# Performance work log

Measured on AMD Instinct MI355X. Metric: run time of the kernel, lower is better.

The kernel has to match this reference:

```python
import jax, jax.numpy as jnp
import numpy as np
import math

B, S, D, H = 2, 2048, 1024, 16
HD = D // H  # head_dim = 64

def setup_inputs() -> dict:
    key = jax.random.key(0)
    ks = jax.random.split(key, 11)
    def n(k, shape, scale=1.0):
        return jax.random.normal(k, shape, dtype=jnp.float32) * scale
    w_scale = 1.0 / math.sqrt(D)
    return {
        "q": n(ks[0], (B, S, D)),
        "k": n(ks[1], (B, S, D)),
        "v": n(ks[2], (B, S, D)),
        "WQ_w": n(ks[3], (D, D), w_scale),
        "WQ_b": n(ks[4], (D,), 0.01),
        "WK_w": n(ks[5], (D, D), w_scale),
        "WK_b": n(ks[6], (D,), 0.01),
        "WV_w": n(ks[7], (D, D), w_scale),
        "WV_b": n(ks[8], (D,), 0.01),
        "Wout_w": n(ks[9], (D, D), w_scale),
        "Wout_b": n(ks[10], (D,), 0.01),
    }

def reference(q, k, v, WQ_w, WQ_b, WK_w, WK_b, WV_w, WV_b, Wout_w, Wout_b):
    b, s, _ = k.shape
    # QKV projections (torch Linear: x @ W.T + b; here weights stored [in, out])
    qh = (q @ WQ_w + WQ_b).reshape(b, -1, H, HD).transpose(0, 2, 1, 3)  # [b,h,s,hd]
    kh = (k @ WK_w + WK_b).reshape(b, -1, H, HD).transpose(0, 2, 1, 3)
    vh = (v @ WV_w + WV_b).reshape(b, -1, H, HD).transpose(0, 2, 1, 3)
    # naive attention: full [b,h,s,s] score matrix
    scores = jnp.einsum("bhqd,bhkd->bhqk", qh, kh) / math.sqrt(HD)
    attn = jax.nn.softmax(scores, axis=-1)
    out = jnp.einsum("bhqk,bhkd->bhqd", attn, vh)
    concat = out.transpose(0, 2, 1, 3).reshape(b, -1, H * HD)  # [b,s,inner_dim]
    return concat @ Wout_w + Wout_b
```

## Files before the change

kernel.cpp:

```cpp
#include <hip/hip_runtime.h>
#include <hip/hip_bf16.h>
#include <stdint.h>

typedef __attribute__((ext_vector_type(8))) short bf16x8;
typedef __attribute__((ext_vector_type(4))) short short4v;
typedef __attribute__((ext_vector_type(4))) float f32x4;

#define MFMA16x16x32 __builtin_amdgcn_mfma_f32_16x16x32_bf16

__device__ __forceinline__ short f2b(float f) {
  union { float f; uint32_t u; } x;
  x.f = f;
  uint32_t u = x.u;
  uint32_t r = (u + 0x7FFFu + ((u >> 16) & 1u)) >> 16;
  return (short)(uint16_t)r;
}

__device__ __forceinline__ uint32_t cvt_pk_bf16(float lo, float hi) {
  uint32_t r;
  asm volatile("v_cvt_pk_bf16_f32 %0, %1, %2" : "=v"(r) : "v"(lo), "v"(hi));
  return r;
}
__device__ __forceinline__ float exp2_fast(float x) {
  float r;
  asm volatile("v_exp_f32 %0, %1" : "=v"(r) : "v"(x));
  return r;
}
__device__ __forceinline__ bf16x8 cvt8(const float4 a, const float4 b) {
  union { uint32_t u[4]; bf16x8 v; } o;
  o.u[0] = cvt_pk_bf16(a.x, a.y);
  o.u[1] = cvt_pk_bf16(a.z, a.w);
  o.u[2] = cvt_pk_bf16(b.x, b.y);
  o.u[3] = cvt_pk_bf16(b.z, b.w);
  return o.v;
}

__device__ __forceinline__ void async_copy16(const void* g, void* l) {
  __builtin_amdgcn_global_load_lds(
      (const __attribute__((address_space(1))) void*)g,
      (__attribute__((address_space(3))) void*)l, 16, 0, 0);
}

__global__ void transpose4_kernel(const float* __restrict__ W0,
                                  const float* __restrict__ W1,
                                  const float* __restrict__ W2,
                                  const float* __restrict__ W3,
                                  short* __restrict__ Wt) {
  __shared__ short tile[64][72];
  const int mat = blockIdx.z;
  const float* W = (mat == 0) ? W0 : (mat == 1) ? W1 : (mat == 2) ? W2 : W3;
  short* Wo = Wt + (size_t)mat * 1024 * 1024;
  const int r0 = blockIdx.y * 64;
  const int c0 = blockIdx.x * 64;
  const int t = threadIdx.x;
#pragma unroll
  for (int i = 0; i < 4; ++i) {
    const int lin = i * 1024 + t * 4;
    const int r = lin >> 6, c = lin & 63;
    const float4 v = *(const float4*)&W[(size_t)(r0 + r) * 1024 + c0 + c];
    tile[r][c + 0] = f2b(v.x);
    tile[r][c + 1] = f2b(v.y);
    tile[r][c + 2] = f2b(v.z);
    tile[r][c + 3] = f2b(v.w);
  }
  __syncthreads();
#pragma unroll
  for (int i = 0; i < 2; ++i) {
    const int lin = i * 2048 + t * 8;
    const int r = lin >> 6, c = lin & 63;
    bf16x8 ov;
#pragma unroll
    for (int jj = 0; jj < 8; ++jj) ov[jj] = tile[c + jj][r];
    *(bf16x8*)&Wo[(size_t)(c0 + r) * 1024 + r0 + c] = ov;
  }
}

__launch_bounds__(256, 2)
__global__ void gemm_qkv_kernel(const float* __restrict__ A0,
                                const float* __restrict__ A1,
                                const float* __restrict__ A2,
                                const short* __restrict__ WtBase,
                                const float* __restrict__ b0,
                                const float* __restrict__ b1,
                                const float* __restrict__ b2,
                                short* __restrict__ C0,
                                short* __restrict__ C1,
                                short* __restrict__ Vt) {
  const int K = 1024;
  __shared__ short As[128 * 64];
  __shared__ short Bs[128 * 64];

  const int y = blockIdx.y;
  const float* A = (y == 0) ? A0 : (y == 1) ? A1 : A2;
  const short* Wt = WtBase + (size_t)y * 1024 * 1024;
  const float* bias = (y == 0) ? b0 : (y == 1) ? b1 : b2;

  const int tm = blockIdx.x & 31;
  const int tn = blockIdx.x >> 5;
  const int m0 = tm * 128, n0 = tn * 128;

  const int tid = threadIdx.x;
  const int lane = tid & 63;
  const int w = tid >> 6;
  const int wr = w >> 1, wc = w & 1;

  const int srow = lane >> 3;
  const int schunk = lane & 7;

  f32x4 acc[4][4] = {};

  for (int kt = 0; kt < 16; ++kt) {
    const int k0 = kt * 64;
#pragma unroll
    for (int i = 0; i < 4; ++i) {
      const int ri = w * 4 + i;
      const int row = ri * 8 + srow;
      const int gch = schunk ^ (row & 7);
      async_copy16(Wt + (size_t)(n0 + row) * K + (k0 + gch * 8), &Bs[ri * 512]);
    }
#pragma unroll
    for (int i = 0; i < 4; ++i) {
      const int ri = w * 4 + i;
      const int row = ri * 8 + srow;
      const float* src = A + (size_t)(m0 + row) * 1024 + k0 + schunk * 8;
      const float4 a = *(const float4*)src;
      const float4 b = *(const float4*)(src + 4);
      *(bf16x8*)&As[row * 64 + ((schunk ^ (row & 7)) << 3)] = cvt8(a, b);
    }
    __syncthreads();
#pragma unroll
    for (int kk = 0; kk < 2; ++kk) {
      bf16x8 af[4], bfr[4];
#pragma unroll
      for (int x = 0; x < 4; ++x) {
        const int gch = kk * 4 + (lane >> 4);
        const int rowA = wr * 64 + x * 16 + (lane & 15);
        af[x] = *(const bf16x8*)&As[rowA * 64 + ((gch ^ (rowA & 7)) << 3)];
        const int rowB = wc * 64 + x * 16 + (lane & 15);
        bfr[x] = *(const bf16x8*)&Bs[rowB * 64 + ((gch ^ (rowB & 7)) << 3)];
      }
#pragma unroll
      for (int x = 0; x < 4; ++x)
#pragma unroll
        for (int yy = 0; yy < 4; ++yy)
          acc[x][yy] = MFMA16x16x32(af[x], bfr[yy], acc[x][yy], 0, 0, 0);
    }
    __syncthreads();
  }

  short* Cout = (y == 0) ? C0 : C1;
#pragma unroll
  for (int x = 0; x < 4; ++x) {
    const int rbase = m0 + wr * 64 + x * 16 + ((lane >> 4) << 2);
#pragma unroll
    for (int yy = 0; yy < 4; ++yy) {
      const int col = n0 + wc * 64 + yy * 16 + (lane & 15);
      const float bv = bias[col];
      if (y == 2) {
        const int b = rbase >> 11, s = rbase & 2047;
        const int hh = col >> 6, d = col & 63;
        short4v pack;
#pragma unroll
        for (int r = 0; r < 4; ++r) pack[r] = f2b(acc[x][yy][r] + bv);
        *(short4v*)&Vt[((size_t)(b * 16 + hh) * 64 + d) * 2048 + s] = pack;
      } else {
#pragma unroll
        for (int r = 0; r < 4; ++r)
          Cout[(size_t)(rbase + r) * 1024 + col] = f2b(acc[x][yy][r] + bv);
      }
    }
  }
}

__launch_bounds__(256, 2)
__global__ void gemm_out_kernel(const short* __restrict__ A,
                                const short* __restrict__ Wt,
                                const float* __restrict__ bias,
                                float* __restrict__ C) {
  const int N = 1024, K = 1024;
  __shared__ short As[128 * 64];
  __shared__ short Bs[128 * 64];

  const int tm = blockIdx.x & 31;
  const int tn = blockIdx.x >> 5;
  const int m0 = tm * 128, n0 = tn * 128;

  const int tid = threadIdx.x;
  const int lane = tid & 63;
  const int w = tid >> 6;
  const int wr = w >> 1, wc = w & 1;
  const int srow = lane >> 3, schunk = lane & 7;

  f32x4 acc[4][4] = {};

  for (int kt = 0; kt < 16; ++kt) {
    const int k0 = kt * 64;
#pragma unroll
    for (int i = 0; i < 4; ++i) {
      const int ri = w * 4 + i;
      const int row = ri * 8 + srow;
      const int gch = schunk ^ (row & 7);
      async_copy16(A + (size_t)(m0 + row) * K + (k0 + gch * 8), &As[ri * 512]);
      async_copy16(Wt + (size_t)(n0 + row) * K + (k0 + gch * 8), &Bs[ri * 512]);
    }
    __syncthreads();
#pragma unroll
    for (int kk = 0; kk < 2; ++kk) {
      bf16x8 af[4], bfr[4];
#pragma unroll
      for (int x = 0; x < 4; ++x) {
        const int gch = kk * 4 + (lane >> 4);
        const int rowA = wr * 64 + x * 16 + (lane & 15);
        af[x] = *(const bf16x8*)&As[rowA * 64 + ((gch ^ (rowA & 7)) << 3)];
        const int rowB = wc * 64 + x * 16 + (lane & 15);
        bfr[x] = *(const bf16x8*)&Bs[rowB * 64 + ((gch ^ (rowB & 7)) << 3)];
      }
#pragma unroll
      for (int x = 0; x < 4; ++x)
#pragma unroll
        for (int yy = 0; yy < 4; ++yy)
          acc[x][yy] = MFMA16x16x32(af[x], bfr[yy], acc[x][yy], 0, 0, 0);
    }
    __syncthreads();
  }

#pragma unroll
  for (int x = 0; x < 4; ++x) {
    const int rbase = m0 + wr * 64 + x * 16 + ((lane >> 4) << 2);
#pragma unroll
    for (int yy = 0; yy < 4; ++yy) {
      const int col = n0 + wc * 64 + yy * 16 + (lane & 15);
      const float bv = bias[col];
#pragma unroll
      for (int r = 0; r < 4; ++r)
        C[(size_t)(rbase + r) * N + col] = acc[x][yy][r] + bv;
    }
  }
}

__launch_bounds__(256, 2)
__global__ void attn_kernel(const short* __restrict__ qh,
                            const short* __restrict__ kh,
                            const short* __restrict__ Vt,
                            short* __restrict__ concat) {
  const int S = 2048;
  const float CL2 = 0.18033688011112042f;
  __shared__ short Ks[2][64 * 64];
  __shared__ short Vs[2][64 * 64];
  __shared__ short Ps[4 * 32 * 64];

  const int qb = blockIdx.x;
  const int h = blockIdx.y;
  const int b = blockIdx.z;
  const int tid = threadIdx.x, lane = tid & 63, w = tid >> 6;
  const int hi = lane >> 4, cc = lane & 15;

  const size_t rowbase = (size_t)b * S;
  const int q0 = qb * 128 + w * 32;

  bf16x8 qf[2][2];
#pragma unroll
  for (int aq = 0; aq < 2; ++aq)
#pragma unroll
    for (int kk = 0; kk < 2; ++kk) {
      const int col = h * 64 + kk * 32 + hi * 8;
      qf[aq][kk] =
          *(const bf16x8*)&qh[(rowbase + q0 + aq * 16 + cc) * 1024 + col];
    }

  f32x4 oacc[2][4] = {};
  float l[2] = {0.f, 0.f};

  const short* Vth = Vt + (size_t)(b * 16 + h) * 64 * 2048;
  short* Pw = &Ps[w * 2048];
  const int srow = lane >> 3, schunk = lane & 7;
  const int e0 = (cc >> 3) & 1;

#pragma unroll
  for (int i = 0; i < 2; ++i) {
    const int ri = w * 2 + i;
    const int row = ri * 8 + srow;
    const int gch = schunk ^ (row & 7);
    async_copy16(&kh[(rowbase + row) * 1024 + h * 64 + gch * 8], &Ks[0][ri * 512]);
    async_copy16(&Vth[(size_t)row * 2048 + gch * 8], &Vs[0][ri * 512]);
  }
  __syncthreads();

  for (int t = 0; t < S / 64; ++t) {
    const int cur = t & 1;
    if (t + 1 < S / 64) {
      const int kv0 = (t + 1) * 64;
#pragma unroll
      for (int i = 0; i < 2; ++i) {
        const int ri = w * 2 + i;
        const int row = ri * 8 + srow;
        const int gch = schunk ^ (row & 7);
        async_copy16(&kh[(rowbase + kv0 + row) * 1024 + h * 64 + gch * 8],
                     &Ks[cur ^ 1][ri * 512]);
        async_copy16(&Vth[(size_t)row * 2048 + kv0 + gch * 8],
                     &Vs[cur ^ 1][ri * 512]);
      }
    }

    f32x4 sacc[2][4] = {};
#pragma unroll
    for (int kk = 0; kk < 2; ++kk) {
      bf16x8 kf[4];
#pragma unroll
      for (int n = 0; n < 4; ++n) {
        const int row = n * 16 + cc;
        const int ch = (kk * 4 + hi) ^ (cc & 7);
        kf[n] = *(const bf16x8*)&Ks[cur][row * 64 + (ch << 3)];
      }
#pragma unroll
      for (int aq = 0; aq < 2; ++aq)
#pragma unroll
        for (int n = 0; n < 4; ++n)
          sacc[aq][n] = MFMA16x16x32(kf[n], qf[aq][kk], sacc[aq][n], 0, 0, 0);
    }

#pragma unroll
    for (int aq = 0; aq < 2; ++aq) {
      const int qrow = aq * 16 + cc;
#pragma unroll
      for (int n = 0; n < 4; ++n) {
        const float p0 = exp2_fast(sacc[aq][n][0] * CL2);
        const float p1 = exp2_fast(sacc[aq][n][1] * CL2);
        const float p2 = exp2_fast(sacc[aq][n][2] * CL2);
        const float p3 = exp2_fast(sacc[aq][n][3] * CL2);
        l[aq] += (p0 + p1) + (p2 + p3);
        const uint32_t u0 = cvt_pk_bf16(p0, p1);
        const uint32_t u1 = cvt_pk_bf16(p2, p3);
        const int chunk = (2 * n + (hi >> 1)) ^ (cc & 7);
        const int base = qrow * 64 + (chunk << 3) + ((hi & 1) << 2);
        *(uint32_t*)&Pw[base + (e0 << 1)] = e0 ? u1 : u0;
        *(uint32_t*)&Pw[base + ((e0 ^ 1) << 1)] = e0 ? u0 : u1;
      }
    }

#pragma unroll
    for (int kvh = 0; kvh < 2; ++kvh) {
      const int ch = (kvh * 4 + hi) ^ (cc & 7);
      bf16x8 pf[2], vf[4];
#pragma unroll
      for (int aq = 0; aq < 2; ++aq)
        pf[aq] = *(const bf16x8*)&Pw[(aq * 16 + cc) * 64 + (ch << 3)];
#pragma unroll
      for (int n = 0; n < 4; ++n) {
        const int row = n * 16 + cc;
        vf[n] = *(const bf16x8*)&Vs[cur][row * 64 + (ch << 3)];
      }
#pragma unroll
      for (int aq = 0; aq < 2; ++aq)
#pragma unroll
        for (int n = 0; n < 4; ++n)
          oacc[aq][n] = MFMA16x16x32(vf[n], pf[aq], oacc[aq][n], 0, 0, 0);
    }
    __syncthreads();
  }

#pragma unroll
  for (int aq = 0; aq < 2; ++aq) {
    float lv = l[aq];
    lv += __shfl_xor(lv, 16);
    lv += __shfl_xor(lv, 32);
    const float inv = 1.0f / lv;
    const size_t grow = rowbase + q0 + aq * 16 + cc;
#pragma unroll
    for (int n = 0; n < 4; ++n)
#pragma unroll
      for (int r = 0; r < 4; ++r) {
        const int d = n * 16 + hi * 4 + r;
        concat[grow * 1024 + h * 64 + d] = f2b(oacc[aq][n][r] * inv);
      }
  }
}

extern "C" void kernel_launch(void* const* d_in, const int* in_sizes, int n_in,
                              void* d_out, int out_size, void* d_ws, size_t ws_size,
                              hipStream_t stream) {
  const float* q = (const float*)d_in[0];
  const float* k = (const float*)d_in[1];
  const float* v = (const float*)d_in[2];
  const float* WQ = (const float*)d_in[3];
  const float* bQ = (const float*)d_in[4];
  const float* WK = (const float*)d_in[5];
  const float* bK = (const float*)d_in[6];
  const float* WV = (const float*)d_in[7];
  const float* bV = (const float*)d_in[8];
  const float* WO = (const float*)d_in[9];
  const float* bO = (const float*)d_in[10];

  char* ws = (char*)d_ws;
  const size_t MB = 1024 * 1024;
  short* Wt = (short*)ws;
  short* qh = (short*)(ws + 8 * MB);
  short* kh = (short*)(ws + 16 * MB);
  short* Vt = (short*)(ws + 24 * MB);
  short* concat = (short*)(ws + 32 * MB);

  transpose4_kernel<<<dim3(16, 16, 4), 256, 0, stream>>>(WQ, WK, WV, WO, Wt);
  gemm_qkv_kernel<<<dim3(256, 3), 256, 0, stream>>>(
      q, k, v, Wt, bQ, bK, bV, qh, kh, Vt);
  attn_kernel<<<dim3(16, 16, 2), 256, 0, stream>>>(qh, kh, Vt, concat);
  gemm_out_kernel<<<256, 256, 0, stream>>>(concat, Wt + 3 * MB, bO,
                                           (float*)d_out);
}
```

Measured before the change: 123.5 us.

## Load GEMM A operand directly to registers and double-buffer weight tiles in LDS

In both the QKV and output projection GEMMs, the A operand is no longer staged through shared memory. Each wave now reads its MFMA fragments straight from global memory (converting fp32 to bf16 in registers for the QKV kernel). The weight tile is double-buffered in LDS, with the next tile prefetched asynchronously after the barrier, so the trailing __syncthreads per k-step can be removed. The aim is to cut LDS traffic and barriers and to overlap weight loads with MFMA work. The cost is that the two waves sharing a row block now fetch the same A data twice from global/L2, and A load latency is no longer hidden by any prefetch.

```diff
diff --git a/kernel.cpp b/kernel.cpp
--- a/kernel.cpp
+++ b/kernel.cpp
@@ -87,8 +87,7 @@
                                 short* __restrict__ C1,
                                 short* __restrict__ Vt) {
   const int K = 1024;
-  __shared__ short As[128 * 64];
-  __shared__ short Bs[128 * 64];
+  __shared__ short Bs[2][128 * 64];
 
   const int y = blockIdx.y;
   const float* A = (y == 0) ? A0 : (y == 1) ? A1 : A2;
@@ -103,58 +102,73 @@
   const int lane = tid & 63;
   const int w = tid >> 6;
   const int wr = w >> 1, wc = w & 1;
+  const int hi = lane >> 4, cc = lane & 15;
 
   const int srow = lane >> 3;
   const int schunk = lane & 7;
 
   f32x4 acc[4][4] = {};
 
+#pragma unroll
+  for (int i = 0; i < 4; ++i) {
+    const int ri = w * 4 + i;
+    const int row = ri * 8 + srow;
+    const int gch = schunk ^ (row & 7);
+    async_copy16(Wt + (size_t)(n0 + row) * K + gch * 8, &Bs[0][ri * 512]);
+  }
+
   for (int kt = 0; kt < 16; ++kt) {
+    const int cur = kt & 1;
     const int k0 = kt * 64;
-#pragma unroll
-    for (int i = 0; i < 4; ++i) {
-      const int ri = w * 4 + i;
-      const int row = ri * 8 + srow;
-      const int gch = schunk ^ (row & 7);
-      async_copy16(Wt + (size_t)(n0 + row) * K + (k0 + gch * 8), &Bs[ri * 512]);
-    }
-#pragma unroll
-    for (int i = 0; i < 4; ++i) {
-      const int ri = w * 4 + i;
-      const int row = ri * 8 + srow;
-      const float* src = A + (size_t)(m0 + row) * 1024 + k0 + schunk * 8;
-      const float4 a = *(const float4*)src;
-      const float4 b = *(const float4*)(src + 4);
-      *(bf16x8*)&As[row * 64 + ((schunk ^ (row & 7)) << 3)] = cvt8(a, b);
-    }
+
+    bf16x8 af[2][4];
+#pragma unroll
+    for (int kk = 0; kk < 2; ++kk)
+#pragma unroll
+      for (int x = 0; x < 4; ++x) {
+        const float* src = A + (size_t)(m0 + wr * 64 + x * 16 + cc) * 1024 +
+                           k0 + kk * 32 + hi * 8;
+        af[kk][x] = cvt8(*(const float4*)src, *(const float4*)(src + 4));
+      }
+
     __syncthreads();
+
+    if (kt < 15) {
+      const int k1 = k0 + 64;
+#pragma unroll
+      for (int i = 0; i < 4; ++i) {
+        const int ri = w * 4 + i;
+        const int row = ri * 8 + srow;
+        const int gch = schunk ^ (row & 7);
+        async_copy16(Wt + (size_t)(n0 + row) * K + (k1 + gch * 8),
+                     &Bs[cur ^ 1][ri * 512]);
+      }
+    }
+
 #pragma unroll
     for (int kk = 0; kk < 2; ++kk) {
-      bf16x8 af[4], bfr[4];
-#pragma unroll
-      for (int x = 0; x < 4; ++x) {
-        const int gch = kk * 4 + (lane >> 4);
-        const int rowA = wr * 64 + x * 16 + (lane & 15);
-        af[x] = *(const bf16x8*)&As[rowA * 64 + ((gch ^ (rowA & 7)) << 3)];
-        const int rowB = wc * 64 + x * 16 + (lane & 15);
-        bfr[x] = *(const bf16x8*)&Bs[rowB * 64 + ((gch ^ (rowB & 7)) << 3)];
+      bf16x8 bfr[4];
+#pragma unroll
+      for (int yy = 0; yy < 4; ++yy) {
+        const int gch = kk * 4 + hi;
+        const int rowB = wc * 64 + yy * 16 + cc;
+        bfr[yy] = *(const bf16x8*)&Bs[cur][rowB * 64 + ((gch ^ (rowB & 7)) << 3)];
       }
 #pragma unroll
       for (int x = 0; x < 4; ++x)
 #pragma unroll
         for (int yy = 0; yy < 4; ++yy)
-          acc[x][yy] = MFMA16x16x32(af[x], bfr[yy], acc[x][yy], 0, 0, 0);
-    }
-    __syncthreads();
+          acc[x][yy] = MFMA16x16x32(af[kk][x], bfr[yy], acc[x][yy], 0, 0, 0);
+    }
   }
 
   short* Cout = (y == 0) ? C0 : C1;
 #pragma unroll
   for (int x = 0; x < 4; ++x) {
-    const int rbase = m0 + wr * 64 + x * 16 + ((lane >> 4) << 2);
+    const int rbase = m0 + wr * 64 + x * 16 + (hi << 2);
 #pragma unroll
     for (int yy = 0; yy < 4; ++yy) {
-      const int col = n0 + wc * 64 + yy * 16 + (lane & 15);
+      const int col = n0 + wc * 64 + yy * 16 + cc;
       const float bv = bias[col];
       if (y == 2) {
         const int b = rbase >> 11, s = rbase & 2047;
@@ -178,8 +192,7 @@
                                 const float* __restrict__ bias,
                                 float* __restrict__ C) {
   const int N = 1024, K = 1024;
-  __shared__ short As[128 * 64];
-  __shared__ short Bs[128 * 64];
+  __shared__ short Bs[2][128 * 64];
 
   const int tm = blockIdx.x & 31;
   const int tn = blockIdx.x >> 5;
@@ -189,47 +202,68 @@
   const int lane = tid & 63;
   const int w = tid >> 6;
   const int wr = w >> 1, wc = w & 1;
+  const int hi = lane >> 4, cc = lane & 15;
   const int srow = lane >> 3, schunk = lane & 7;
 
   f32x4 acc[4][4] = {};
 
+#pragma unroll
+  for (int i = 0; i < 4; ++i) {
+    const int ri = w * 4 + i;
+    const int row = ri * 8 + srow;
+    const int gch = schunk ^ (row & 7);
+    async_copy16(Wt + (size_t)(n0 + row) * K + gch * 8, &Bs[0][ri * 512]);
+  }
+
   for (int kt = 0; kt < 16; ++kt) {
+    const int cur = kt & 1;
     const int k0 = kt * 64;
-#pragma unroll
-    for (int i = 0; i < 4; ++i) {
-      const int ri = w * 4 + i;
-      const int row = ri * 8 + srow;
-      const int gch = schunk ^ (row & 7);
-      async_copy16(A + (size_t)(m0 + row) * K + (k0 + gch * 8), &As[ri * 512]);
-      async_copy16(Wt + (size_t)(n0 + row) * K + (k0 + gch * 8), &Bs[ri * 512]);
-    }
+
+    bf16x8 af[2][4];
+#pragma unroll
+    for (int kk = 0; kk < 2; ++kk)
+#pragma unroll
+      for (int x = 0; x < 4; ++x)
+        af[kk][x] = *(const bf16x8*)&A[(size_t)(m0 + wr * 64 + x * 16 + cc) * 1024 +
+                                       k0 + kk * 32 + hi * 8];
+
     __syncthreads();
+
+    if (kt < 15) {
+      const int k1 = k0 + 64;
+#pragma unroll
+      for (int i = 0; i < 4; ++i) {
+        const int ri = w * 4 + i;
+        const int row = ri * 8 + srow;
+        const int gch = schunk ^ (row & 7);
+        async_copy16(Wt + (size_t)(n0 + row) * K + (k1 + gch * 8),
+                     &Bs[cur ^ 1][ri * 512]);
+      }
+    }
+
 #pragma unroll
     for (int kk = 0; kk < 2; ++kk) {
-      bf16x8 af[4], bfr[4];
-#pragma unroll
-      for (int x = 0; x < 4; ++x) {
-        const int gch = kk * 4 + (lane >> 4);
-        const int rowA = wr * 64 + x * 16 + (lane & 15);
-        af[x] = *(const bf16x8*)&As[rowA * 64 + ((gch ^ (rowA & 7)) << 3)];
-        const int rowB = wc * 64 + x * 16 + (lane & 15);
-        bfr[x] = *(const bf16x8*)&Bs[rowB * 64 + ((gch ^ (rowB & 7)) << 3)];
+      bf16x8 bfr[4];
+#pragma unroll
+      for (int yy = 0; yy < 4; ++yy) {
+        const int gch = kk * 4 + hi;
+        const int rowB = wc * 64 + yy * 16 + cc;
+        bfr[yy] = *(const bf16x8*)&Bs[cur][rowB * 64 + ((gch ^ (rowB & 7)) << 3)];
       }
 #pragma unroll
       for (int x = 0; x < 4; ++x)
 #pragma unroll
         for (int yy = 0; yy < 4; ++yy)
-          acc[x][yy] = MFMA16x16x32(af[x], bfr[yy], acc[x][yy], 0, 0, 0);
-    }
-    __syncthreads();
+          acc[x][yy] = MFMA16x16x32(af[kk][x], bfr[yy], acc[x][yy], 0, 0, 0);
+    }
   }
 
 #pragma unroll
   for (int x = 0; x < 4; ++x) {
-    const int rbase = m0 + wr * 64 + x * 16 + ((lane >> 4) << 2);
+    const int rbase = m0 + wr * 64 + x * 16 + (hi << 2);
 #pragma unroll
     for (int yy = 0; yy < 4; ++yy) {
-      const int col = n0 + wc * 64 + yy * 16 + (lane & 15);
+      const int col = n0 + wc * 64 + yy * 16 + cc;
       const float bv = bias[col];
 #pragma unroll
       for (int r = 0; r < 4; ++r)
```

After: 188.4 us. 1.53x slower.
